# Performance work log

Hardware: AMD Instinct MI355X
Metric: run time of the kernel (lower is better)

The kernel has to match this reference:

```python
import jax, jax.numpy as jnp
import numpy as np

MAX_DEPTH = 5
BS = 512
D = 32000          # decoder_outdim (non-EOS tokens)
V = D + 1          # + EOS column (eos_token_id == V-1)
ALPHA = 0.1


def setup_inputs() -> dict:
    key = jax.random.key(0)
    k1, k2, k3, k4, k5 = jax.random.split(key, 5)
    # Generators return log-probabilities -> normalize random logits.
    logp_pos = jax.nn.log_softmax(jax.random.normal(k1, (MAX_DEPTH, BS, V), jnp.float32), -1)
    logp_neg = jax.nn.log_softmax(jax.random.normal(k2, (MAX_DEPTH, BS, V), jnp.float32), -1)
    logp_q = jax.nn.log_softmax(jax.random.normal(k3, (MAX_DEPTH, BS, V), jnp.float32), -1)
    # Gumbel noise for multinomial sampling (over the D non-EOS tokens).
    u = jax.random.uniform(k4, (MAX_DEPTH, BS, D), jnp.float32, 1e-6, 1.0 - 1e-6)
    gumbel = -jnp.log(-jnp.log(u))
    # torch.randint(0, 3, (bs,)) per depth
    sampling_target = jax.random.randint(k5, (MAX_DEPTH, BS), 0, 3)
    return {"logp_pos": logp_pos, "logp_neg": logp_neg, "logp_q": logp_q,
            "gumbel": gumbel, "sampling_target": sampling_target}


def _loss(logp_pos, logp_neg, logp_q, gumbel, sampling_target):
    sg = jax.lax.stop_gradient
    dt = logp_pos.dtype
    max_depth, bs, v = logp_pos.shape
    d = v - 1
    eos = v - 1
    ar = jnp.arange(bs)

    # kl_target[j] : depth-dependent target distribution, width V
    denom = jnp.array([sum(d ** i for i in range(j + 1))
                       for j in range(max_depth, 0, -1)], dtype=dt)
    a = 1.0 / denom                                    # (max_depth,)
    kl_target = jnp.concatenate(
        [jnp.broadcast_to(((1.0 - a) / d)[:, None], (max_depth, d)), a[:, None]], -1)

    log_cur = jnp.zeros((bs, 3), dt)   # accumulated log prob of sampled path
    u_seq = jnp.ones((bs,), dt)
    middles, lasts, kls, sms, us = [], [], [], [], []

    for depth in range(max_depth):
        lp, ln, lq = logp_pos[depth], logp_neg[depth], logp_q[depth]
        lpq_sg = sg(lp + lq)

        # middle term
        middle = jnp.sum(
            jnp.exp(lpq_sg) * (1.0 - jnp.exp(sg(ln)))
            * (jnp.sum(log_cur, -1, keepdims=True) + lp + lq), -1)

        # last term (stable sum-except-current, all detached except ln factor)
        m = jnp.max(lpq_sg, -1)
        sum_except = (jnp.sum(jnp.exp(lpq_sg - m[:, None]), -1)
                      * jnp.exp(m))[:, None] - jnp.exp(lpq_sg)
        last = jnp.sum(jnp.exp(sg(ln)) * sum_except * ln, -1)

        # sample next tokens: pick one of {pos,neg,query} per row, then
        # multinomial over exp(logp[:, :-1]) via Gumbel-max
        st = sampling_target[depth]
        sel = jnp.stack([lp[:, :-1], ln[:, :-1], lq[:, :-1]])[st, ar]  # (bs, D)
        nxt = jnp.argmax(sel + gumbel[depth], -1)                      # (bs,)

        lp_n, ln_n, lq_n = lp[ar, nxt], ln[ar, nxt], lq[ar, nxt]
        log_cur = log_cur + jnp.stack([lp_n, ln_n, lq_n], axis=1)

        # KLDivLoss(batchmean): mean_b sum_v t*(log t - x)
        t = kl_target[depth]
        kl = sum(jnp.mean(jnp.sum(t * (jnp.log(t) - x), -1)) for x in (lp, ln, lq))

        sm_stack = sg(jnp.stack([ln_n + lq_n, lp_n + lq_n, lp_n + ln_n]))  # (3, bs)
        sm = jnp.exp(sm_stack[st, ar])

        middles.append(middle); lasts.append(last); kls.append(kl)
        sms.append(sm); us.append(u_seq)
        u_seq = (nxt != eos).astype(dt) * u_seq

    # unfold the recursion from the deepest level
    R = jnp.zeros((bs,), dt)
    for depth in reversed(range(max_depth)):
        base = middles[depth] + lasts[depth] - ALPHA * kls[depth]
        if depth == max_depth - 1:
            R = sg(us[depth]) * base
        else:
            R = sg(us[depth]) * (R * sms[depth] + base)
    return -jnp.mean(R)


def reference(logp_pos, logp_neg, logp_q, gumbel, sampling_target):
    return _loss(logp_pos, logp_neg, logp_q, gumbel, sampling_target)
```

## Files before the change

### kernel.cpp

```cpp
#include <hip/hip_runtime.h>
#include <math.h>

#define MAXDEPTH 5
#define BSZ 512
#define DD 32000
#define VV (DD + 1)
#define ALPHA 0.1f

__device__ __forceinline__ void depth_target(int depth, float* a_out, float* tne_out) {
    double dd = (double)DD;
    double denom = 0.0, p = 1.0;
    const int top = MAXDEPTH - depth;
    for (int i = 0; i <= top; ++i) { denom += p; p *= dd; }
    const float a = (float)(1.0 / denom);
    *a_out = a;
    *tne_out = (1.0f - a) / (float)DD;
}

__global__ __launch_bounds__(256) void pgr_pass1(
    const float* __restrict__ lp_all, const float* __restrict__ ln_all,
    const float* __restrict__ lq_all, const float* __restrict__ gm_all,
    const int* __restrict__ st_all, float* __restrict__ ws)
{
    const int bid = blockIdx.x;
    const int tid = threadIdx.x;
    const size_t off = (size_t)bid;
    const float* __restrict__ lp  = lp_all + off * VV;
    const float* __restrict__ lnv = ln_all + off * VV;
    const float* __restrict__ lq  = lq_all + off * VV;
    const float* __restrict__ gm  = gm_all + off * (size_t)DD;
    const int st = st_all[bid];

    float S1 = 0.f, S2 = 0.f, T = 0.f, A = 0.f, B = 0.f, KL = 0.f;
    float amax = -INFINITY;
    int aidx = 0x7fffffff;

    for (int i = tid; i < DD / 4; i += 256) {
        const float4 p4 = ((const float4*)lp)[i];
        const float4 n4 = ((const float4*)lnv)[i];
        const float4 q4 = ((const float4*)lq)[i];
        const float4 g4 = ((const float4*)gm)[i];
        const float pv[4] = {p4.x, p4.y, p4.z, p4.w};
        const float nv[4] = {n4.x, n4.y, n4.z, n4.w};
        const float qv[4] = {q4.x, q4.y, q4.z, q4.w};
        const float gv[4] = {g4.x, g4.y, g4.z, g4.w};
#pragma unroll
        for (int k = 0; k < 4; ++k) {
            const float lpq = pv[k] + qv[k];
            const float e1 = __expf(lpq);
            const float e2 = __expf(nv[k]);
            const float w  = e1 * (1.f - e2);
            S1 += w;
            S2 += w * lpq;
            T  += e1;
            A  += e2 * nv[k];
            B  += e2 * e1 * nv[k];
            KL += pv[k] + nv[k] + qv[k];
            const float sel = (st == 0) ? pv[k] : ((st == 1) ? nv[k] : qv[k]);
            const float sv  = sel + gv[k];
            if (sv > amax) { amax = sv; aidx = i * 4 + k; }
        }
    }

    const int lane = tid & 63;
    const int wv   = tid >> 6;
#pragma unroll
    for (int o = 32; o > 0; o >>= 1) {
        S1 += __shfl_down(S1, o);
        S2 += __shfl_down(S2, o);
        T  += __shfl_down(T, o);
        A  += __shfl_down(A, o);
        B  += __shfl_down(B, o);
        KL += __shfl_down(KL, o);
        const float ov = __shfl_down(amax, o);
        const int   oi = __shfl_down(aidx, o);
        if (ov > amax || (ov == amax && oi < aidx)) { amax = ov; aidx = oi; }
    }

    __shared__ float sh[4][7];
    __shared__ int   shi[4];
    if (lane == 0) {
        sh[wv][0] = S1; sh[wv][1] = S2; sh[wv][2] = T; sh[wv][3] = A;
        sh[wv][4] = B;  sh[wv][5] = KL; sh[wv][6] = amax;
        shi[wv] = aidx;
    }
    __syncthreads();

    if (tid == 0) {
        for (int w2 = 1; w2 < 4; ++w2) {
            S1 += sh[w2][0]; S2 += sh[w2][1]; T += sh[w2][2];
            A  += sh[w2][3]; B  += sh[w2][4]; KL += sh[w2][5];
            const float ov = sh[w2][6]; const int oi = shi[w2];
            if (ov > amax || (ov == amax && oi < aidx)) { amax = ov; aidx = oi; }
        }
        const float pe = lp[DD], ne = lnv[DD], qe = lq[DD];
        {
            const float lpq = pe + qe;
            const float e1 = __expf(lpq);
            const float e2 = __expf(ne);
            const float w  = e1 * (1.f - e2);
            S1 += w; S2 += w * lpq; T += e1; A += e2 * ne; B += e2 * e1 * ne;
        }
        const float kleos = pe + ne + qe;
        const float last  = T * A - B;

        const int nxt   = aidx;
        const float lpn = lp[nxt], lnn = lnv[nxt], lqn = lq[nxt];
        const float sum3n = lpn + lnn + lqn;
        const float smlog = (st == 0) ? (lnn + lqn)
                          : (st == 1) ? (lpn + lqn)
                                      : (lpn + lnn);
        const float sm = __expf(smlog);

        const int depth = bid / BSZ;
        float a, tne;
        depth_target(depth, &a, &tne);
        const float klrow = tne * KL + a * kleos;

        float* o = ws + (size_t)bid * 6;
        o[0] = S1; o[1] = S2; o[2] = last; o[3] = klrow; o[4] = sm; o[5] = sum3n;
    }
}

__global__ __launch_bounds__(BSZ) void pgr_pass2(
    const float* __restrict__ ws, float* __restrict__ out)
{
    const int r = threadIdx.x;
    __shared__ float red[BSZ];
    __shared__ float klmean_sh;

    float base[MAXDEPTH], smv[MAXDEPTH];
    float logcur = 0.f;

    for (int depth = 0; depth < MAXDEPTH; ++depth) {
        const float* o = ws + ((size_t)depth * BSZ + r) * 6;
        const float S1 = o[0], S2 = o[1], last = o[2];
        const float klrow = o[3], sm = o[4], sum3n = o[5];

        red[r] = klrow;
        __syncthreads();
        for (int s = BSZ / 2; s > 0; s >>= 1) {
            if (r < s) red[r] += red[r + s];
            __syncthreads();
        }
        if (r == 0) klmean_sh = red[0] / (float)BSZ;
        __syncthreads();
        const float klmean = klmean_sh;
        __syncthreads();

        float a, tne;
        depth_target(depth, &a, &tne);
        const float C = (float)DD * tne * logf(tne) + a * logf(a);
        const float kl = 3.f * C - klmean;

        const float mid = S1 * logcur + S2;
        base[depth] = mid + last - ALPHA * kl;
        smv[depth]  = sm;
        logcur += sum3n;
    }

    float R = base[MAXDEPTH - 1];
    for (int depth = MAXDEPTH - 2; depth >= 0; --depth)
        R = R * smv[depth] + base[depth];

    red[r] = R;
    __syncthreads();
    for (int s = BSZ / 2; s > 0; s >>= 1) {
        if (r < s) red[r] += red[r + s];
        __syncthreads();
    }
    if (r == 0) out[0] = -red[0] / (float)BSZ;
}

extern "C" void kernel_launch(void* const* d_in, const int* in_sizes, int n_in,
                              void* d_out, int out_size, void* d_ws, size_t ws_size,
                              hipStream_t stream) {
    const float* lp = (const float*)d_in[0];
    const float* ln = (const float*)d_in[1];
    const float* lq = (const float*)d_in[2];
    const float* gm = (const float*)d_in[3];
    const int*   st = (const int*)d_in[4];
    float* ws  = (float*)d_ws;
    float* out = (float*)d_out;

    pgr_pass1<<<MAXDEPTH * BSZ, 256, 0, stream>>>(lp, ln, lq, gm, st, ws);
    pgr_pass2<<<1, BSZ, 0, stream>>>(ws, out);
}
```

Baseline: 242.2 us.

## Split each row into chunks across persistent blocks and merge partials in pass2

Each (depth,row) is split into four column chunks processed by a fixed grid of 2048 blocks looping over units, with a 2-way unrolled float4 load loop for more memory-level parallelism. Partial sums (reformulated as T,U,P,Q,A,B so S1/S2 are derived later) and argmax candidates go to workspace and are merged in pass2, which also does the EOS and sampled-token gathers. This aims to better saturate HBM bandwidth, at the cost of extra per-unit block syncs and more serial work in the single-block second pass.

```diff
diff --git a/kernel.cpp b/kernel.cpp
--- a/kernel.cpp
+++ b/kernel.cpp
@@ -6,6 +6,13 @@
 #define DD 32000
 #define VV (DD + 1)
 #define ALPHA 0.1f
+
+#define SPLIT 4
+#define CHUNK (DD / SPLIT)
+#define CVEC  (CHUNK / 4)
+#define GRID1 2048
+#define UPB   ((MAXDEPTH * BSZ * SPLIT) / GRID1)
+#define WSS   10
 
 __device__ __forceinline__ void depth_target(int depth, float* a_out, float* tne_out) {
     double dd = (double)DD;
@@ -22,140 +29,176 @@
     const float* __restrict__ lq_all, const float* __restrict__ gm_all,
     const int* __restrict__ st_all, float* __restrict__ ws)
 {
-    const int bid = blockIdx.x;
     const int tid = threadIdx.x;
-    const size_t off = (size_t)bid;
-    const float* __restrict__ lp  = lp_all + off * VV;
-    const float* __restrict__ lnv = ln_all + off * VV;
-    const float* __restrict__ lq  = lq_all + off * VV;
-    const float* __restrict__ gm  = gm_all + off * (size_t)DD;
-    const int st = st_all[bid];
-
-    float S1 = 0.f, S2 = 0.f, T = 0.f, A = 0.f, B = 0.f, KL = 0.f;
-    float amax = -INFINITY;
-    int aidx = 0x7fffffff;
-
-    for (int i = tid; i < DD / 4; i += 256) {
-        const float4 p4 = ((const float4*)lp)[i];
-        const float4 n4 = ((const float4*)lnv)[i];
-        const float4 q4 = ((const float4*)lq)[i];
-        const float4 g4 = ((const float4*)gm)[i];
-        const float pv[4] = {p4.x, p4.y, p4.z, p4.w};
-        const float nv[4] = {n4.x, n4.y, n4.z, n4.w};
-        const float qv[4] = {q4.x, q4.y, q4.z, q4.w};
-        const float gv[4] = {g4.x, g4.y, g4.z, g4.w};
+    const int lane = tid & 63;
+    const int wv = tid >> 6;
+    __shared__ float sh[4][9];
+    __shared__ int shi[4];
+
+    const int u0 = blockIdx.x * UPB;
+    for (int uu = 0; uu < UPB; ++uu) {
+        const int u = u0 + uu;
+        const int dr = u / SPLIT;
+        const int s = u % SPLIT;
+        const size_t rowoff = (size_t)dr * VV;
+        const float* __restrict__ lp  = lp_all + rowoff + (size_t)s * CHUNK;
+        const float* __restrict__ lnv = ln_all + rowoff + (size_t)s * CHUNK;
+        const float* __restrict__ lq  = lq_all + rowoff + (size_t)s * CHUNK;
+        const float* __restrict__ gm  = gm_all + (size_t)dr * DD + (size_t)s * CHUNK;
+        const int st = st_all[dr];
+        const int gbase = s * CHUNK;
+
+        float T = 0.f, U = 0.f, P = 0.f, Q = 0.f, A = 0.f, B = 0.f, KL = 0.f;
+        float amax = -INFINITY;
+        int aidx = 0x7fffffff;
+
+#define ELEM(pv, nv, qv, gv, gidx) do {                                   \
+        const float lpq = (pv) + (qv);                                    \
+        KL += lpq + (nv);                                                 \
+        const float e1 = __expf(lpq);                                     \
+        const float e2 = __expf(nv);                                      \
+        const float e12 = e1 * e2;                                        \
+        T += e1; U += e12;                                                \
+        P = fmaf(e1, lpq, P); Q = fmaf(e12, lpq, Q);                      \
+        A = fmaf(e2, (nv), A); B = fmaf(e12, (nv), B);                    \
+        const float sel = (st == 0) ? (pv) : ((st == 1) ? (nv) : (qv));   \
+        const float sv = sel + (gv);                                      \
+        if (sv > amax) { amax = sv; aidx = (gidx); }                      \
+    } while (0)
+
+        for (int i = tid; i < CVEC; i += 512) {
+            const int j = i + 256;
+            const bool jb = (j < CVEC);
+            const float4 pa = ((const float4*)lp)[i];
+            const float4 na = ((const float4*)lnv)[i];
+            const float4 qa = ((const float4*)lq)[i];
+            const float4 ga = ((const float4*)gm)[i];
+            float4 pb, nb, qb, gb;
+            if (jb) {
+                pb = ((const float4*)lp)[j];
+                nb = ((const float4*)lnv)[j];
+                qb = ((const float4*)lq)[j];
+                gb = ((const float4*)gm)[j];
+            }
+            ELEM(pa.x, na.x, qa.x, ga.x, gbase + i * 4 + 0);
+            ELEM(pa.y, na.y, qa.y, ga.y, gbase + i * 4 + 1);
+            ELEM(pa.z, na.z, qa.z, ga.z, gbase + i * 4 + 2);
+            ELEM(pa.w, na.w, qa.w, ga.w, gbase + i * 4 + 3);
+            if (jb) {
+                ELEM(pb.x, nb.x, qb.x, gb.x, gbase + j * 4 + 0);
+                ELEM(pb.y, nb.y, qb.y, gb.y, gbase + j * 4 + 1);
+                ELEM(pb.z, nb.z, qb.z, gb.z, gbase + j * 4 + 2);
+                ELEM(pb.w, nb.w, qb.w, gb.w, gbase + j * 4 + 3);
+            }
+        }
+#undef ELEM
+
 #pragma unroll
-        for (int k = 0; k < 4; ++k) {
-            const float lpq = pv[k] + qv[k];
-            const float e1 = __expf(lpq);
-            const float e2 = __expf(nv[k]);
-            const float w  = e1 * (1.f - e2);
-            S1 += w;
-            S2 += w * lpq;
-            T  += e1;
-            A  += e2 * nv[k];
-            B  += e2 * e1 * nv[k];
-            KL += pv[k] + nv[k] + qv[k];
-            const float sel = (st == 0) ? pv[k] : ((st == 1) ? nv[k] : qv[k]);
-            const float sv  = sel + gv[k];
-            if (sv > amax) { amax = sv; aidx = i * 4 + k; }
-        }
+        for (int o = 32; o > 0; o >>= 1) {
+            T += __shfl_down(T, o); U += __shfl_down(U, o);
+            P += __shfl_down(P, o); Q += __shfl_down(Q, o);
+            A += __shfl_down(A, o); B += __shfl_down(B, o);
+            KL += __shfl_down(KL, o);
+            const float ov = __shfl_down(amax, o);
+            const int oi = __shfl_down(aidx, o);
+            if (ov > amax || (ov == amax && oi < aidx)) { amax = ov; aidx = oi; }
+        }
+        if (lane == 0) {
+            sh[wv][0] = T; sh[wv][1] = U; sh[wv][2] = P; sh[wv][3] = Q;
+            sh[wv][4] = A; sh[wv][5] = B; sh[wv][6] = KL; sh[wv][7] = amax;
+            shi[wv] = aidx;
+        }
+        __syncthreads();
+        if (tid == 0) {
+            for (int w2 = 1; w2 < 4; ++w2) {
+                T += sh[w2][0]; U += sh[w2][1]; P += sh[w2][2]; Q += sh[w2][3];
+                A += sh[w2][4]; B += sh[w2][5]; KL += sh[w2][6];
+                const float ov = sh[w2][7]; const int oi = shi[w2];
+                if (ov > amax || (ov == amax && oi < aidx)) { amax = ov; aidx = oi; }
+            }
+            float* o = ws + (size_t)u * WSS;
+            o[0] = T; o[1] = U; o[2] = P; o[3] = Q; o[4] = A; o[5] = B;
+            o[6] = KL; o[7] = amax; o[8] = __int_as_float(aidx);
+        }
+        __syncthreads();
     }
-
-    const int lane = tid & 63;
-    const int wv   = tid >> 6;
+}
+
+__global__ __launch_bounds__(BSZ) void pgr_pass2(
+    const float* __restrict__ ws,
+    const float* __restrict__ lp_all, const float* __restrict__ ln_all,
+    const float* __restrict__ lq_all, const int* __restrict__ st_all,
+    float* __restrict__ out)
+{
+    const int r = threadIdx.x;
+    __shared__ float red[BSZ];
+    __shared__ float klmean_sh;
+
+    float base[MAXDEPTH], smv[MAXDEPTH];
+    float logcur = 0.f;
+
+    for (int depth = 0; depth < MAXDEPTH; ++depth) {
+        const int dr = depth * BSZ + r;
+        float T = 0.f, U = 0.f, P = 0.f, Q = 0.f, A = 0.f, B = 0.f, KL = 0.f;
+        float amax = -INFINITY;
+        int aidx = 0x7fffffff;
 #pragma unroll
-    for (int o = 32; o > 0; o >>= 1) {
-        S1 += __shfl_down(S1, o);
-        S2 += __shfl_down(S2, o);
-        T  += __shfl_down(T, o);
-        A  += __shfl_down(A, o);
-        B  += __shfl_down(B, o);
-        KL += __shfl_down(KL, o);
-        const float ov = __shfl_down(amax, o);
-        const int   oi = __shfl_down(aidx, o);
-        if (ov > amax || (ov == amax && oi < aidx)) { amax = ov; aidx = oi; }
-    }
-
-    __shared__ float sh[4][7];
-    __shared__ int   shi[4];
-    if (lane == 0) {
-        sh[wv][0] = S1; sh[wv][1] = S2; sh[wv][2] = T; sh[wv][3] = A;
-        sh[wv][4] = B;  sh[wv][5] = KL; sh[wv][6] = amax;
-        shi[wv] = aidx;
-    }
-    __syncthreads();
-
-    if (tid == 0) {
-        for (int w2 = 1; w2 < 4; ++w2) {
-            S1 += sh[w2][0]; S2 += sh[w2][1]; T += sh[w2][2];
-            A  += sh[w2][3]; B  += sh[w2][4]; KL += sh[w2][5];
-            const float ov = sh[w2][6]; const int oi = shi[w2];
+        for (int s = 0; s < SPLIT; ++s) {
+            const float* o = ws + ((size_t)dr * SPLIT + s) * WSS;
+            T += o[0]; U += o[1]; P += o[2]; Q += o[3];
+            A += o[4]; B += o[5]; KL += o[6];
+            const float ov = o[7]; const int oi = __float_as_int(o[8]);
             if (ov > amax || (ov == amax && oi < aidx)) { amax = ov; aidx = oi; }
         }
-        const float pe = lp[DD], ne = lnv[DD], qe = lq[DD];
+
+        const size_t rowoff = (size_t)dr * VV;
+        const float pe = lp_all[rowoff + DD];
+        const float ne = ln_all[rowoff + DD];
+        const float qe = lq_all[rowoff + DD];
         {
             const float lpq = pe + qe;
             const float e1 = __expf(lpq);
             const float e2 = __expf(ne);
-            const float w  = e1 * (1.f - e2);
-            S1 += w; S2 += w * lpq; T += e1; A += e2 * ne; B += e2 * e1 * ne;
-        }
+            const float e12 = e1 * e2;
+            T += e1; U += e12;
+            P = fmaf(e1, lpq, P); Q = fmaf(e12, lpq, Q);
+            A = fmaf(e2, ne, A); B = fmaf(e12, ne, B);
+        }
+        const float S1 = T - U;
+        const float S2 = P - Q;
+        const float last = T * A - B;
         const float kleos = pe + ne + qe;
-        const float last  = T * A - B;
-
-        const int nxt   = aidx;
-        const float lpn = lp[nxt], lnn = lnv[nxt], lqn = lq[nxt];
+
+        float a, tne;
+        depth_target(depth, &a, &tne);
+        const float klrow = tne * KL + a * kleos;
+
+        red[r] = klrow;
+        __syncthreads();
+        for (int s = BSZ / 2; s > 0; s >>= 1) {
+            if (r < s) red[r] += red[r + s];
+            __syncthreads();
+        }
+        if (r == 0) klmean_sh = red[0] / (float)BSZ;
+        __syncthreads();
+        const float klmean = klmean_sh;
+        __syncthreads();
+
+        const float C = (float)DD * tne * logf(tne) + a * logf(a);
+        const float kl = 3.f * C - klmean;
+
+        const int nxt = aidx;
+        const float lpn = lp_all[rowoff + nxt];
+        const float lnn = ln_all[rowoff + nxt];
+        const float lqn = lq_all[rowoff + nxt];
         const float sum3n = lpn + lnn + lqn;
+        const int st = st_all[dr];
         const float smlog = (st == 0) ? (lnn + lqn)
                           : (st == 1) ? (lpn + lqn)
                                       : (lpn + lnn);
-        const float sm = __expf(smlog);
-
-        const int depth = bid / BSZ;
-        float a, tne;
-        depth_target(depth, &a, &tne);
-        const float klrow = tne * KL + a * kleos;
-
-        float* o = ws + (size_t)bid * 6;
-        o[0] = S1; o[1] = S2; o[2] = last; o[3] = klrow; o[4] = sm; o[5] = sum3n;
-    }
-}
-
-__global__ __launch_bounds__(BSZ) void pgr_pass2(
-    const float* __restrict__ ws, float* __restrict__ out)
-{
-    const int r = threadIdx.x;
-    __shared__ float red[BSZ];
-    __shared__ float klmean_sh;
-
-    float base[MAXDEPTH], smv[MAXDEPTH];
-    float logcur = 0.f;
-
-    for (int depth = 0; depth < MAXDEPTH; ++depth) {
-        const float* o = ws + ((size_t)depth * BSZ + r) * 6;
-        const float S1 = o[0], S2 = o[1], last = o[2];
-        const float klrow = o[3], sm = o[4], sum3n = o[5];
-
-        red[r] = klrow;
-        __syncthreads();
-        for (int s = BSZ / 2; s > 0; s >>= 1) {
-            if (r < s) red[r] += red[r + s];
-            __syncthreads();
-        }
-        if (r == 0) klmean_sh = red[0] / (float)BSZ;
-        __syncthreads();
-        const float klmean = klmean_sh;
-        __syncthreads();
-
-        float a, tne;
-        depth_target(depth, &a, &tne);
-        const float C = (float)DD * tne * logf(tne) + a * logf(a);
-        const float kl = 3.f * C - klmean;
-
-        const float mid = S1 * logcur + S2;
-        base[depth] = mid + last - ALPHA * kl;
-        smv[depth]  = sm;
+
+        base[depth] = S1 * logcur + S2 + last - ALPHA * kl;
+        smv[depth] = __expf(smlog);
         logcur += sum3n;
     }
 
@@ -183,6 +226,6 @@
     float* ws  = (float*)d_ws;
     float* out = (float*)d_out;
 
-    pgr_pass1<<<MAXDEPTH * BSZ, 256, 0, stream>>>(lp, ln, lq, gm, st, ws);
-    pgr_pass2<<<1, BSZ, 0, stream>>>(ws, out);
-}
+    pgr_pass1<<<GRID1, 256, 0, stream>>>(lp, ln, lq, gm, st, ws);
+    pgr_pass2<<<1, BSZ, 0, stream>>>(ws, lp, ln, lq, st, out);
+}
```

After: 282.5 us. 16.7% more time.
